# Optimization experiments

Measured on AMD Instinct MI355X. Metric: run time of the kernel, lower is better.

The kernel has to match this reference:

```python
import jax, jax.numpy as jnp
import numpy as np

# module hyper-params (init_kwargs); shift_sz=1 => 1x1 patches == pixels, flag == mask
SHIFT_SZ = 1
STRIDE = 1
MASK_THRED = 1
TRIPLE_WEIGHT = 1.0   # only rescales gradients in the original custom backward; forward output unchanged
FUSE = True
FUSE_K = 3            # contextual-attention fuse kernel size (identity 3x3)


def _fuse_scores(score, H, W):
    # score: [B, L, L] (query loc, key loc). Contextual-attention 'fuse':
    # smooth the score map with an identity kernel along both spatial unfoldings.
    B, L, _ = score.shape
    eye = jnp.eye(FUSE_K, dtype=score.dtype).reshape(1, 1, FUSE_K, FUSE_K)

    def conv(x):
        return jax.lax.conv_general_dilated(
            x, eye, window_strides=(1, 1), padding='SAME',
            dimension_numbers=('NCHW', 'OIHW', 'NCHW'))

    s = conv(score[:, None])                                            # [B,1,L,L]
    s = s.reshape(B, H, W, H, W).transpose(0, 2, 1, 4, 3).reshape(B, 1, L, L)
    s = conv(s)
    s = s.reshape(B, W, H, W, H).transpose(0, 2, 1, 4, 3).reshape(B, L, L)
    return s


def reference(x, mask):
    # x: [B, 2c, H, W]; first c channels = former (decoder feat), last c = latter (encoder feat)
    B, C2, H, W = x.shape
    c = C2 // 2
    L = H * W
    former = x[:, :c]
    latter = x[:, c:]

    # flag: True = inside hole. With shift_sz=1, stride=1, mask_thred=1 the patch flag is the mask itself.
    flag = mask.reshape(L) > 0.5                                        # [L]

    lat = latter.reshape(B, c, L)
    # normalize context (key) patches to unit L2 norm -> cosine-style correlation
    key = lat / jnp.maximum(jnp.linalg.norm(lat, axis=1, keepdims=True), 1e-4)
    score = jnp.einsum('bcl,bck->blk', lat, key)                        # [B, L(query), L(key)]
    if FUSE:
        score = _fuse_scores(score, H, W)

    # only attend to context patches OUTSIDE the hole
    score = jnp.where(flag[None, None, :], -jnp.inf, score)
    attn = jax.nn.softmax(score, axis=-1)                               # [B, L, L]

    # soft shift: attention-weighted gather of former (decoder) features from context pixels
    shift = jnp.einsum('blk,bck->bcl', attn, former.reshape(B, c, L))   # [B, c, L]
    # the shifted feature only fills hole locations; zero elsewhere
    shift = shift * flag[None, None, :].astype(x.dtype)
    shift = shift.reshape(B, c, H, W)

    return jnp.concatenate([former, latter, shift], axis=1)             # [B, 3c, H, W]


def setup_inputs():
    key = jax.random.key(0)
    k1, k2 = jax.random.split(key)
    B, c, H, W = 2, 64, 64, 64
    x = jax.random.normal(k1, (B, 2 * c, H, W), dtype=jnp.float32)
    mask = (jax.random.uniform(k2, (1, 1, H, W)) > 0.75).astype(jnp.float32)
    return {"x": x, "mask": mask}
```

## Files before the change

kernel.cpp:

```cpp
#include <hip/hip_runtime.h>
#include <math.h>


#define L 4096

typedef unsigned int   u32;
typedef unsigned short u16;
typedef short  short8 __attribute__((ext_vector_type(8)));
typedef float  f32x16 __attribute__((ext_vector_type(16)));

#define MFMA32(a, b, c) __builtin_amdgcn_mfma_f32_32x32x16_bf16((a), (b), (c), 0, 0, 0)

__device__ __forceinline__ u16 f2bf(float f) {
    u32 u = __float_as_uint(f);
    u32 r = (u + 0x7FFFu + ((u >> 16) & 1u)) >> 16;
    return (u16)r;
}

__device__ __forceinline__ void lds_async16(void* lds, const void* g) {
    __builtin_amdgcn_global_load_lds((const __attribute__((address_space(1))) u32*)g,
                                     (__attribute__((address_space(3))) u32*)lds, 16, 0, 0);
}

#define OFF_LATB  0u
#define OFF_FORB  1048576u
#define OFF_GARR  2097152u
#define GARR_BB   1575936u
#define OFF_FBITS 5249024u
#define OFF_ROWS  5249536u
#define OFF_CNT   5265920u
#define OFF_PART  5266432u
#define OFF_KNB   5266432u

__global__ void k_pre1(const float4* __restrict__ x4, float4* __restrict__ out4,
                       const float* __restrict__ x, const float* __restrict__ mask,
                       u16* __restrict__ latb, u16* __restrict__ knb, u16* __restrict__ forb,
                       int* __restrict__ rows, int* __restrict__ cnt, u32* __restrict__ fbits)
{
    const int blk = blockIdx.x, t = threadIdx.x;
    if (blk < 1537) {
        int i = blk * 256 + t;
        if (i < 262144) {
            int b = i >> 17, j = i & 131071;
            out4[b * 196608 + j] = x4[b * 131072 + j];
        } else if (i < 393216) {
            int z = i - 262144; int b = z >> 16, j = z & 65535;
            out4[b * 196608 + 131072 + j] = make_float4(0.f, 0.f, 0.f, 0.f);
        }
    } else if (blk < 1569) {
        int tid = (blk - 1537) * 256 + t;
        int b = tid >> 12, l = tid & 4095;
        const float* xb = x + (size_t)b * 524288;
        float v[64]; float ss = 0.f;
        #pragma unroll
        for (int c = 0; c < 64; ++c) { v[c] = xb[(64 + c) * 4096 + l]; ss += v[c] * v[c]; }
        float inv = 1.f / fmaxf(sqrtf(ss), 1e-4f);
        u16* lr = latb + (size_t)(b * 4096 + l) * 64;
        u16* kr = knb  + (size_t)(b * 4096 + l) * 64;
        #pragma unroll
        for (int c8 = 0; c8 < 8; ++c8) {
            u32 wl[4], wk[4];
            #pragma unroll
            for (int i = 0; i < 4; ++i) {
                float a = v[c8 * 8 + 2 * i], bb2 = v[c8 * 8 + 2 * i + 1];
                wl[i] = (u32)f2bf(a) | ((u32)f2bf(bb2) << 16);
                wk[i] = (u32)f2bf(a * inv) | ((u32)f2bf(bb2 * inv) << 16);
            }
            uint4 pl = make_uint4(wl[0], wl[1], wl[2], wl[3]);
            uint4 pk = make_uint4(wk[0], wk[1], wk[2], wk[3]);
            *(uint4*)(lr + c8 * 8) = pl;
            *(uint4*)(kr + c8 * 8) = pk;
        }
        u16* fr = forb + (size_t)(b * 4096 + l) * 64;
        #pragma unroll
        for (int c8 = 0; c8 < 8; ++c8) {
            u32 wf[4];
            #pragma unroll
            for (int i = 0; i < 4; ++i) {
                float a = xb[(c8 * 8 + 2 * i) * 4096 + l];
                float bb2 = xb[(c8 * 8 + 2 * i + 1) * 4096 + l];
                wf[i] = (u32)f2bf(a) | ((u32)f2bf(bb2) << 16);
            }
            uint4 pf = make_uint4(wf[0], wf[1], wf[2], wf[3]);
            *(uint4*)(fr + c8 * 8) = pf;
        }
    } else {
        __shared__ int lcnt;
        __shared__ u32 lb[128];
        if (t == 0) lcnt = 0;
        if (t < 128) lb[t] = 0u;
        __syncthreads();
        for (int i = t; i < L; i += 256) {
            if (mask[i] > 0.5f) {
                int p = atomicAdd(&lcnt, 1); rows[p] = i;
                int kp = ((i & 63) << 6) | (i >> 6);
                atomicOr(&lb[kp >> 5], 1u << (kp & 31));
            }
        }
        __syncthreads();
        if (t < 128) fbits[t] = lb[t];
        if (t == 0) cnt[0] = lcnt;
    }
}

__global__ void k_garr(const u16* __restrict__ knb, char* __restrict__ garr)
{
    int tid = blockIdx.x * 256 + threadIdx.x;
    if (tid >= 2 * 4104 * 3) return;
    int b = tid / 12312; int rem = tid - b * 12312;
    int sg = rem / 3, aa = rem - 3 * (rem / 3);
    int mp = sg - 1;
    char* dst = garr + (size_t)b * GARR_BB + (size_t)sg * 384;
    int key = (sg & 7) << 4;
    const u16* src = nullptr;
    if (mp >= 0 && mp < L) {
        int q = (((mp & 63) << 6) | (mp >> 6)) + aa - 1;
        if (q >= 0 && q < L) src = knb + (size_t)b * 262144 + (size_t)q * 64;
    }
    #pragma unroll
    for (int c8 = 0; c8 < 8; ++c8) {
        uint4 v = src ? *(const uint4*)(src + c8 * 8) : make_uint4(0, 0, 0, 0);
        *(uint4*)(dst + ((aa * 128 + c8 * 16) ^ key)) = v;
    }
}

__global__ __launch_bounds__(256, 2)
void k_flash(const u16* __restrict__ latb, const u16* __restrict__ forb,
             const char* __restrict__ garr, const u32* __restrict__ fbits,
             const int* __restrict__ rows, const int* __restrict__ cnt,
             char* __restrict__ part)
{
    __shared__ __align__(16) char smem[80000];
    char* slab = smem;
    u16*  F_s  = (u16*)(smem + 52224);
    u16*  p_s  = (u16*)(smem + 69632);
    int*  rl_s = (int*)(smem + 79872);

    const int t = threadIdx.x;
    const int rt = blockIdx.x, ks = blockIdx.y, b = blockIdx.z;
    const int count = cnt[0];
    const int base = rt * 32;
    if (base >= count) return;
    const int nact = min(32, count - base);
    if (t < 32) rl_s[t] = rows[base + min(t, nact - 1)];
    __syncthreads();

    const int l = t & 63, w = t >> 6;
    const int li = l & 31, hi = l >> 5;
    const size_t boff = (size_t)b * 262144;

    const u16* zp = (const u16*)garr;
    int gl = rl_s[li];
    int tl0 = ((gl & 63) << 6) | (gl >> 6);
    const u16* rp[9];
    #pragma unroll
    for (int tap = 0; tap < 9; ++tap) {
        int bb = tap / 3, aa = tap - 3 * (tap / 3);
        int mp = tl0 + bb - 1;
        const u16* p = zp;
        if (mp >= 0 && mp < L) {
            int q = (((mp & 63) << 6) | (mp >> 6)) + aa - 1;
            if (q >= 0 && q < L) p = latb + boff + (size_t)q * 64;
        }
        rp[tap] = p;
    }
    short8 bu[36];
    #pragma unroll
    for (int q = 0; q < 36; ++q) {
        int tap = q >> 2, Ksi = q & 3;
        bu[q] = *(const short8*)(rp[tap] + Ksi * 16 + hi * 8);
    }

    float mrun = -INFINITY, srun = 0.f;
    f32x16 acc0, acc1;
    #pragma unroll
    for (int r = 0; r < 16; ++r) { acc0[r] = 0.f; acc1[r] = 0.f; }

    const int kp0 = ks * 512;
    const char* gb = garr + (size_t)b * GARR_BB;

    for (int kt = 0; kt < 4; ++kt) {
        const int k0p = kp0 + kt * 128;
        __syncthreads();

        const char* gw = gb + (size_t)k0p * 384;
        #pragma unroll
        for (int i = 0; i < 13; ++i) {
            int idx = w + 4 * i;
            if (idx < 51)
                lds_async16(slab + idx * 1024, gw + idx * 1024 + l * 16);
        }

        {
            int kpA = k0p + 2 * l, kpB = kpA + 1;
            int kA = ((kpA & 63) << 6) | (kpA >> 6);
            int kB = ((kpB & 63) << 6) | (kpB >> 6);
            const u32* pa = (const u32*)(forb + boff + (size_t)kA * 64 + w * 16);
            const u32* pc = (const u32*)(forb + boff + (size_t)kB * 64 + w * 16);
            uint4 A0 = *(const uint4*)pa, A1 = *(const uint4*)(pa + 4);
            uint4 B0 = *(const uint4*)pc, B1 = *(const uint4*)(pc + 4);
            u32 av[8] = {A0.x, A0.y, A0.z, A0.w, A1.x, A1.y, A1.z, A1.w};
            u32 bv[8] = {B0.x, B0.y, B0.z, B0.w, B1.x, B1.y, B1.z, B1.w};
            #pragma unroll
            for (int i2 = 0; i2 < 8; ++i2) {
                u32 w0 = (av[i2] & 0xffffu) | (bv[i2] << 16);
                u32 w1 = (av[i2] >> 16) | (bv[i2] & 0xffff0000u);
                *(u32*)((char*)F_s + (w * 16 + 2 * i2) * 272 + l * 4) = w0;
                *(u32*)((char*)F_s + (w * 16 + 2 * i2 + 1) * 272 + l * 4) = w1;
            }
        }
        asm volatile("s_waitcnt vmcnt(0)" ::: "memory");
        __syncthreads();

        f32x16 sc;
        #pragma unroll
        for (int r = 0; r < 16; ++r) sc[r] = 0.f;
        const int slot_base = w * 32 + li;
        #pragma unroll
        for (int tap = 0; tap < 9; ++tap) {
            int bb = tap / 3, aa = tap - 3 * (tap / 3);
            int sl = slot_base + bb;
            int key = (sl & 7) << 4;
            int base_b = sl * 384 + aa * 128 + hi * 16;
            #pragma unroll
            for (int Ksi = 0; Ksi < 4; ++Ksi) {
                short8 ag = *(const short8*)(slab + ((base_b + Ksi * 32) ^ key));
                sc = MFMA32(ag, bu[tap * 4 + Ksi], sc);
            }
        }

        u32 bits = fbits[(k0p >> 5) + w];
        float sv[16]; float mx = -INFINITY;
        #pragma unroll
        for (int r = 0; r < 16; ++r) {
            int kloc = (r & 3) + 8 * (r >> 2) + 4 * hi;
            float s = sc[r];
            if ((bits >> kloc) & 1) s = -INFINITY;
            sv[r] = s; mx = fmaxf(mx, s);
        }
        mx = fmaxf(mx, __shfl_xor(mx, 32, 64));
        float newm = fmaxf(mrun, mx);
        float fac, tsum = 0.f;
        u16 pb[16];
        if (newm > -INFINITY) {
            fac = __expf(mrun - newm);
            #pragma unroll
            for (int r = 0; r < 16; ++r) { float p = __expf(sv[r] - newm); tsum += p; pb[r] = f2bf(p); }
        } else {
            fac = 1.f;
            #pragma unroll
            for (int r = 0; r < 16; ++r) pb[r] = 0;
        }
        tsum += __shfl_xor(tsum, 32, 64);
        srun = srun * fac + tsum;
        mrun = newm;
        #pragma unroll
        for (int rq = 0; rq < 8; ++rq) {
            int r = rq * 2;
            int kloc = (r & 3) + 8 * (r >> 2) + 4 * hi;
            u32 pw = (u32)pb[r] | ((u32)pb[r + 1] << 16);
            *(u32*)(p_s + w * 1280 + li * 40 + kloc) = pw;
        }

        #pragma unroll
        for (int r = 0; r < 16; ++r) {
            int row = (r & 3) + 8 * (r >> 2) + 4 * hi;
            float fr = __shfl(fac, row, 64);
            acc0[r] *= fr; acc1[r] *= fr;
        }
        #pragma unroll
        for (int Ksi2 = 0; Ksi2 < 2; ++Ksi2) {
            short8 pa2 = *(const short8*)(p_s + w * 1280 + li * 40 + Ksi2 * 16 + hi * 8);
            short8 f0 = *(const short8*)(F_s + li * 136 + w * 32 + Ksi2 * 16 + hi * 8);
            short8 f1 = *(const short8*)(F_s + (32 + li) * 136 + w * 32 + Ksi2 * 16 + hi * 8);
            acc0 = MFMA32(pa2, f0, acc0);
            acc1 = MFMA32(pa2, f1, acc1);
        }
    }

    __syncthreads();
    float* um = (float*)smem;
    if (l < 32) { um[(w * 32 + li) * 66] = mrun; um[(w * 32 + li) * 66 + 1] = srun; }
    #pragma unroll
    for (int r = 0; r < 16; ++r) {
        int row = (r & 3) + 8 * (r >> 2) + 4 * hi;
        um[(w * 32 + row) * 66 + 2 + li] = acc0[r];
        um[(w * 32 + row) * 66 + 2 + 32 + li] = acc1[r];
    }
    __syncthreads();
    {
        int row = t >> 3, cq = t & 7;
        float m4[4], s4[4];
        #pragma unroll
        for (int wv = 0; wv < 4; ++wv) {
            m4[wv] = um[(wv * 32 + row) * 66];
            s4[wv] = um[(wv * 32 + row) * 66 + 1];
        }
        float M = fmaxf(fmaxf(m4[0], m4[1]), fmaxf(m4[2], m4[3]));
        float S = 0.f; float wx[4];
        if (M > -INFINITY) {
            #pragma unroll
            for (int wv = 0; wv < 4; ++wv) { wx[wv] = __expf(m4[wv] - M); S += s4[wv] * wx[wv]; }
        } else {
            wx[0] = wx[1] = wx[2] = wx[3] = 0.f;
        }
        char* pp = part + ((size_t)((b * 128 + rt) * 8 + ks)) * 4608 + row * 144;
        u16 h[8];
        #pragma unroll
        for (int i = 0; i < 8; ++i) {
            int ch = cq * 8 + i;
            float v = 0.f;
            #pragma unroll
            for (int wv = 0; wv < 4; ++wv) v += wx[wv] * um[(wv * 32 + row) * 66 + 2 + ch];
            h[i] = f2bf(v);
        }
        if (cq == 0) { *(float*)pp = M; *(float*)(pp + 4) = S; }
        uint4 hw;
        hw.x = (u32)h[0] | ((u32)h[1] << 16); hw.y = (u32)h[2] | ((u32)h[3] << 16);
        hw.z = (u32)h[4] | ((u32)h[5] << 16); hw.w = (u32)h[6] | ((u32)h[7] << 16);
        *(uint4*)(pp + 16 + cq * 16) = hw;
    }
}

__global__ void k_reduce(const int* __restrict__ rows, const int* __restrict__ cnt,
                         const char* __restrict__ part, float* __restrict__ out)
{
    int t = threadIdx.x;
    int row = t >> 3, cq = t & 7;
    int rt = blockIdx.x, b = blockIdx.y;
    int count = cnt[0];
    int slot = rt * 32 + row;
    if (slot >= count) return;
    int l = rows[slot];
    const char* pb = part + ((size_t)((b * 128 + rt) * 8)) * 4608 + row * 144;
    float M = -INFINITY, m8[8], s8[8];
    #pragma unroll
    for (int k = 0; k < 8; ++k) {
        m8[k] = *(const float*)(pb + k * 4608);
        s8[k] = *(const float*)(pb + k * 4608 + 4);
        M = fmaxf(M, m8[k]);
    }
    if (!(M > -INFINITY)) return;
    float S = 0.f; float accv[8] = {0.f, 0.f, 0.f, 0.f, 0.f, 0.f, 0.f, 0.f};
    #pragma unroll
    for (int k = 0; k < 8; ++k) {
        float wxv = __expf(m8[k] - M);
        S += s8[k] * wxv;
        uint4 hv = *(const uint4*)(pb + k * 4608 + 16 + cq * 16);
        u32 uu[4] = {hv.x, hv.y, hv.z, hv.w};
        #pragma unroll
        for (int i = 0; i < 4; ++i) {
            accv[2 * i]     += wxv * __uint_as_float((uu[i] & 0xffffu) << 16);
            accv[2 * i + 1] += wxv * __uint_as_float(uu[i] & 0xffff0000u);
        }
    }
    float inv = (S > 0.f) ? 1.f / S : 0.f;
    float* ob = out + (size_t)b * 786432 + 524288 + l;
    #pragma unroll
    for (int i = 0; i < 8; ++i) ob[(size_t)(cq * 8 + i) * 4096] = accv[i] * inv;
}

extern "C" void kernel_launch(void* const* d_in, const int* in_sizes, int n_in,
                              void* d_out, int out_size, void* d_ws, size_t ws_size,
                              hipStream_t stream)
{
    const float* x    = (const float*)d_in[0];
    const float* mask = (const float*)d_in[1];
    float* out = (float*)d_out;
    char* ws = (char*)d_ws;

    u16* latb = (u16*)(ws + OFF_LATB);
    u16* forb = (u16*)(ws + OFF_FORB);
    char* garr = ws + OFF_GARR;
    u32* fbits = (u32*)(ws + OFF_FBITS);
    int* rows  = (int*)(ws + OFF_ROWS);
    int* cnt   = (int*)(ws + OFF_CNT);
    char* part = ws + OFF_PART;
    u16* knb   = (u16*)(ws + OFF_KNB);

    k_pre1<<<1570, 256, 0, stream>>>((const float4*)x, (float4*)out, x, mask,
                                     latb, knb, forb, rows, cnt, fbits);
    k_garr<<<97, 256, 0, stream>>>(knb, garr);
    k_flash<<<dim3(128, 8, 2), 256, 0, stream>>>(latb, forb, garr, fbits, rows, cnt, part);
    k_reduce<<<dim3(128, 2), 256, 0, stream>>>(rows, cnt, part, out);
}
```

Baseline: 143.7 us.

## Rewrite attention pipeline: fuse reduce into flash kernel, drop gather-array pass

Most of the pipeline is replaced. The separate k_garr gather kernel goes away, and k_pre1 now writes normalized keys straight into a swizzled, transposed padded layout plus a channel-major former buffer via an LDS transpose. k_flash now uses 512 threads and large dynamic LDS, each block covering a 512-key slice in one pass without online-softmax rescaling. The last block to finish each row tile, found through an atomic done counter, does the cross-split reduction in place of the k_reduce launch. It also remaps blocks across XCDs and caps hole rows at 2048; in exchange it brings atomics, threadfences and lower occupancy.

```diff
diff --git a/kernel.cpp b/kernel.cpp
--- a/kernel.cpp
+++ b/kernel.cpp
@@ -3,361 +3,345 @@
 
 
 #define L 4096
-
 typedef unsigned int   u32;
 typedef unsigned short u16;
 typedef short  short8 __attribute__((ext_vector_type(8)));
 typedef float  f32x16 __attribute__((ext_vector_type(16)));
 
-#define MFMA32(a, b, c) __builtin_amdgcn_mfma_f32_32x32x16_bf16((a), (b), (c), 0, 0, 0)
-
-__device__ __forceinline__ u16 f2bf(float f) {
-    u32 u = __float_as_uint(f);
-    u32 r = (u + 0x7FFFu + ((u >> 16) & 1u)) >> 16;
-    return (u16)r;
+#define MFMA32(a,b,c) __builtin_amdgcn_mfma_f32_32x32x16_bf16((a),(b),(c),0,0,0)
+
+__device__ __forceinline__ u16 f2bf(float f){ u32 u=__float_as_uint(f); return (u16)((u+0x7FFFu+((u>>16)&1u))>>16); }
+__device__ __forceinline__ u32 pack2(float a, float b){ return (u32)f2bf(a) | ((u32)f2bf(b)<<16); }
+__device__ __forceinline__ void lds_async16(void* lds, const void* g){
+  __builtin_amdgcn_global_load_lds((const __attribute__((address_space(1))) u32*)g,
+                                   (__attribute__((address_space(3))) u32*)lds, 16, 0, 0);
 }
 
-__device__ __forceinline__ void lds_async16(void* lds, const void* g) {
-    __builtin_amdgcn_global_load_lds((const __attribute__((address_space(1))) u32*)g,
-                                     (__attribute__((address_space(3))) u32*)lds, 16, 0, 0);
-}
-
 #define OFF_LATB  0u
-#define OFF_FORB  1048576u
-#define OFF_GARR  2097152u
-#define GARR_BB   1575936u
-#define OFF_FBITS 5249024u
-#define OFF_ROWS  5249536u
-#define OFF_CNT   5265920u
-#define OFF_PART  5266432u
-#define OFF_KNB   5266432u
+#define OFF_FORKP 1048576u
+#define OFF_KNXG  2097152u
+#define KNXG_BB   542208u
+#define OFF_FBITS 3211264u
+#define OFF_ROWS  3211776u
+#define OFF_CNT   3228160u
+#define OFF_DONE  3228416u
+#define OFF_PART  3229440u
+
+#define SLAB_O  0
+#define POFF    82432
+#define ZOFF    90624
+#define UOFF    90752
+#define PSOFF   127616
+#define RLOFF   162432
+#define SMEM_SZ 162688
 
 __global__ void k_pre1(const float4* __restrict__ x4, float4* __restrict__ out4,
                        const float* __restrict__ x, const float* __restrict__ mask,
-                       u16* __restrict__ latb, u16* __restrict__ knb, u16* __restrict__ forb,
-                       int* __restrict__ rows, int* __restrict__ cnt, u32* __restrict__ fbits)
+                       u16* __restrict__ latb, u16* __restrict__ forkp,
+                       char* __restrict__ knxg, int* __restrict__ rows,
+                       int* __restrict__ cnt, u32* __restrict__ fbits,
+                       u32* __restrict__ done)
 {
+    __shared__ float tl[64*65];
+    __shared__ int lcnt;
+    __shared__ u32 lb[128];
     const int blk = blockIdx.x, t = threadIdx.x;
-    if (blk < 1537) {
-        int i = blk * 256 + t;
-        if (i < 262144) {
-            int b = i >> 17, j = i & 131071;
-            out4[b * 196608 + j] = x4[b * 131072 + j];
-        } else if (i < 393216) {
-            int z = i - 262144; int b = z >> 16, j = z & 65535;
-            out4[b * 196608 + 131072 + j] = make_float4(0.f, 0.f, 0.f, 0.f);
-        }
-    } else if (blk < 1569) {
-        int tid = (blk - 1537) * 256 + t;
-        int b = tid >> 12, l = tid & 4095;
-        const float* xb = x + (size_t)b * 524288;
-        float v[64]; float ss = 0.f;
-        #pragma unroll
-        for (int c = 0; c < 64; ++c) { v[c] = xb[(64 + c) * 4096 + l]; ss += v[c] * v[c]; }
-        float inv = 1.f / fmaxf(sqrtf(ss), 1e-4f);
-        u16* lr = latb + (size_t)(b * 4096 + l) * 64;
-        u16* kr = knb  + (size_t)(b * 4096 + l) * 64;
-        #pragma unroll
-        for (int c8 = 0; c8 < 8; ++c8) {
-            u32 wl[4], wk[4];
+    if (blk < 1536) {
+        int i = blk*256 + t;
+        if (i < 262144) { int b=i>>17, j=i&131071; out4[b*196608+j] = x4[b*131072+j]; }
+        else { int z=i-262144; int b=z>>16, j=z&65535; out4[b*196608+131072+j] = make_float4(0.f,0.f,0.f,0.f); }
+    } else if (blk < 1568) {
+        int tid = (blk-1536)*256+t; int b = tid>>12, l = tid&4095;
+        const float* xb = x + (size_t)b*524288;
+        float v[64]; float ss=0.f;
+        #pragma unroll
+        for (int c=0;c<64;++c){ v[c]=xb[(64+c)*4096+l]; ss+=v[c]*v[c]; }
+        float inv = 1.f/fmaxf(sqrtf(ss),1e-4f);
+        u16* lr = latb + (size_t)(b*4096+l)*64;
+        #pragma unroll
+        for (int c8=0;c8<8;++c8){
+            uint4 pq = make_uint4(pack2(v[c8*8],v[c8*8+1]),pack2(v[c8*8+2],v[c8*8+3]),
+                                  pack2(v[c8*8+4],v[c8*8+5]),pack2(v[c8*8+6],v[c8*8+7]));
+            *(uint4*)(lr + c8*8) = pq;
+        }
+        int t2 = ((l&63)<<6)|(l>>6);
+        char* dst = knxg + (size_t)b*KNXG_BB + (size_t)(t2+66)*128;
+        int key = (t2&7)<<4;
+        #pragma unroll
+        for (int c8=0;c8<8;++c8){
+            uint4 pq = make_uint4(pack2(v[c8*8]*inv,v[c8*8+1]*inv),pack2(v[c8*8+2]*inv,v[c8*8+3]*inv),
+                                  pack2(v[c8*8+4]*inv,v[c8*8+5]*inv),pack2(v[c8*8+6]*inv,v[c8*8+7]*inv));
+            *(uint4*)(dst + ((c8*16)^key)) = pq;
+        }
+    } else if (blk < 1696) {
+        int blk2 = blk-1568; int b = blk2>>6, ch = blk2&63;
+        const float* in = x + (size_t)b*524288 + (size_t)ch*4096;
+        #pragma unroll
+        for (int i=0;i<16;++i){ int idx = t+256*i; tl[(idx&63)*65 + (idx>>6)] = in[idx]; }
+        __syncthreads();
+        u32* orow = (u32*)forkp + (size_t)(b*64+ch)*2048;
+        #pragma unroll
+        for (int i=0;i<8;++i){
+            int j2 = t+256*i; int j = 2*j2;
+            float f0 = tl[(j>>6)*65 + (j&63)];
+            float f1 = tl[((j+1)>>6)*65 + ((j+1)&63)];
+            orow[j2] = pack2(f0,f1);
+        }
+    } else if (blk < 1698) {
+        int b = blk-1696;
+        char* gB = knxg + (size_t)b*KNXG_BB;
+        uint4 z = make_uint4(0,0,0,0);
+        #pragma unroll
+        for (int i=0;i<5;++i){
+            int idx = t+256*i;
+            if (idx < 1120){
+                int row = (idx<528) ? (idx>>3) : (4162 + ((idx-528)>>3));
+                *(uint4*)(gB + (size_t)row*128 + (idx&7)*16) = z;
+            }
+        }
+    } else {
+        if (t==0) lcnt=0;
+        if (t<128) lb[t]=0u;
+        __syncthreads();
+        for (int i=t;i<L;i+=256){
+            if (mask[i] > 0.5f){
+                int p = atomicAdd(&lcnt,1);
+                if (p<2048) rows[p]=i;
+                int kp = ((i&63)<<6)|(i>>6);
+                atomicOr(&lb[kp>>5], 1u<<(kp&31));
+            }
+        }
+        __syncthreads();
+        if (t<128) fbits[t]=lb[t];
+        if (t<128) done[t]=0u;
+        if (t==0) cnt[0]=min(lcnt,2048);
+    }
+}
+
+__global__ __launch_bounds__(512,1)
+void k_flash(const u16* __restrict__ latb, const u16* __restrict__ forkp,
+             const char* __restrict__ knxg, const u32* __restrict__ fbits,
+             const int* __restrict__ rows, const int* __restrict__ cnt,
+             char* __restrict__ part, u32* __restrict__ done, float* __restrict__ out)
+{
+    extern __shared__ char smem[];
+    const int t = threadIdx.x;
+    const int lin = blockIdx.x;
+    const int xcd = lin&7, qd = lin>>3;
+    const int gid = xcd*128 + qd;
+    const int ksb = gid>>6, rt = gid&63;
+    const int ks = ksb>>1, b = ksb&1;
+    const int count = cnt[0];
+    const int base = rt*32;
+    if (base >= count) return;
+    const int nact = min(32, count-base);
+    int* rl_s = (int*)(smem + RLOFF);
+    if (t < 32) rl_s[t] = rows[base + min(t, nact-1)];
+    if (t < 8) *(uint4*)(smem + ZOFF + t*16) = make_uint4(0,0,0,0);
+    __syncthreads();
+
+    const int l = t&63, w = t>>6, li = l&31, hi = l>>5;
+    const int k0 = ks*512, wOff = w*64;
+    const int plo = (ks==0) ? 4031 : 1;
+    const char* slabsrc = knxg + (size_t)b*KNXG_BB + (size_t)k0*128;
+
+    #pragma unroll
+    for (int i=0;i<11;++i){
+        int idx = w + 8*i;
+        if (idx < 80 || (idx == 80 && l < 24))
+            lds_async16(smem + SLAB_O + idx*1024, slabsrc + idx*1024 + l*16);
+    }
+    if (ks==0 || ks==7){
+        const char* psrc = knxg + (size_t)b*KNXG_BB + (size_t)(plo+66)*128;
+        lds_async16(smem + POFF + w*1024, psrc + w*1024 + l*16);
+    }
+    {
+        const u16* latbb = latb + (size_t)b*262144;
+        int gl = rl_s[li];
+        int tl0 = ((gl&63)<<6)|(gl>>6);
+        #pragma unroll
+        for (int rep=0;rep<5;++rep){
+            int f = w + 8*rep;
+            if (f < 36){
+                int tap = f>>2, Ks = f&3;
+                int bb = tap/3, aa = tap - 3*bb;
+                int mp = tl0 + bb - 1;
+                short8 val = {0,0,0,0,0,0,0,0};
+                if (mp>=0 && mp<L){
+                    int qq = (((mp&63)<<6)|(mp>>6)) + aa - 1;
+                    if (qq>=0 && qq<L)
+                        val = *(const short8*)(latbb + (size_t)qq*64 + Ks*16 + hi*8);
+                }
+                *(short8*)(smem + UOFF + f*1024 + l*16) = val;
+            }
+        }
+    }
+    int pkA[2][9];
+    #pragma unroll
+    for (int Mt=0; Mt<2; ++Mt){
+        #pragma unroll
+        for (int tap=0; tap<9; ++tap){
+            const int bb = tap/3, aa = tap - 3*(tap/3);
+            int j = k0 + wOff + Mt*32 + li + bb - 1;
+            int pk = ZOFF;
+            if ((u32)j < (u32)L){
+                int qq = (j&63)*64 + (j>>6) + aa - 1;
+                if ((u32)qq < (u32)L){
+                    int t2 = ((qq&63)<<6) | (qq>>6);
+                    int key = (t2&7)<<4;
+                    int s = t2 - k0 + 66;
+                    if ((u32)s < 643u) pk = SLAB_O + s*128 + key;
+                    else               pk = POFF + (t2 - plo)*128 + key;
+                }
+            }
+            pkA[Mt][tap] = pk;
+        }
+    }
+
+    asm volatile("s_waitcnt vmcnt(0)" ::: "memory");
+    __syncthreads();
+
+    f32x16 sc0, sc1;
+    #pragma unroll
+    for (int r=0;r<16;++r){ sc0[r]=0.f; sc1[r]=0.f; }
+    const char* ubp = smem + UOFF + l*16;
+    const int X0 = hi*16;
+    __builtin_amdgcn_s_setprio(1);
+    #pragma unroll
+    for (int tap=0; tap<9; ++tap){
+        const int r0 = pkA[0][tap] & ~127, y0 = pkA[0][tap] & 127;
+        const int r1 = pkA[1][tap] & ~127, y1 = pkA[1][tap] & 127;
+        #pragma unroll
+        for (int Ks=0; Ks<4; ++Ks){
+            short8 bu = *(const short8*)(ubp + (tap*4+Ks)*1024);
+            short8 a0 = *(const short8*)(smem + r0 + ((X0 + Ks*32) ^ y0));
+            short8 a1 = *(const short8*)(smem + r1 + ((X0 + Ks*32) ^ y1));
+            sc0 = MFMA32(a0, bu, sc0);
+            sc1 = MFMA32(a1, bu, sc1);
+        }
+    }
+    __builtin_amdgcn_s_setprio(0);
+
+    const u16* fKb = forkp + (size_t)b*262144;
+    short8 fb0[4], fb1[4];
+    #pragma unroll
+    for (int Ks=0;Ks<4;++Ks){
+        fb0[Ks] = *(const short8*)(fKb + (size_t)li*4096      + k0 + wOff + Ks*16 + hi*8);
+        fb1[Ks] = *(const short8*)(fKb + (size_t)(32+li)*4096 + k0 + wOff + Ks*16 + hi*8);
+    }
+
+    const int fw = (k0 + wOff) >> 5;
+    const u32 bits0 = fbits[fw], bits1 = fbits[fw+1];
+    float mx = -INFINITY;
+    #pragma unroll
+    for (int r=0;r<16;++r){
+        int kl = (r&3) + 8*(r>>2) + 4*hi;
+        float s0 = sc0[r]; if ((bits0>>kl)&1u) s0 = -INFINITY;
+        float s1 = sc1[r]; if ((bits1>>kl)&1u) s1 = -INFINITY;
+        sc0[r]=s0; sc1[r]=s1;
+        mx = fmaxf(mx, fmaxf(s0,s1));
+    }
+    mx = fmaxf(mx, __shfl_xor(mx, 32, 64));
+    float sum = 0.f;
+    u32 pw0[8], pw1[8];
+    if (mx > -INFINITY){
+        #pragma unroll
+        for (int rq=0;rq<8;++rq){
+            float p00 = __expf(sc0[2*rq]-mx), p01 = __expf(sc0[2*rq+1]-mx);
+            float p10 = __expf(sc1[2*rq]-mx), p11 = __expf(sc1[2*rq+1]-mx);
+            sum += (p00+p01)+(p10+p11);
+            pw0[rq] = pack2(p00,p01);
+            pw1[rq] = pack2(p10,p11);
+        }
+    } else {
+        #pragma unroll
+        for (int rq=0;rq<8;++rq){ pw0[rq]=0u; pw1[rq]=0u; }
+    }
+    sum += __shfl_xor(sum, 32, 64);
+    char* pswr = smem + PSOFF + w*4352 + li*136;
+    #pragma unroll
+    for (int rq=0;rq<8;++rq){
+        int r = 2*rq;
+        int kl = (r&3) + 8*(r>>2) + 4*hi;
+        *(u32*)(pswr + kl*2)      = pw0[rq];
+        *(u32*)(pswr + 64 + kl*2) = pw1[rq];
+    }
+
+    f32x16 ac0, ac1;
+    #pragma unroll
+    for (int r=0;r<16;++r){ ac0[r]=0.f; ac1[r]=0.f; }
+    #pragma unroll
+    for (int Ks=0;Ks<4;++Ks){
+        short8 pa = *(const short8*)(pswr + Ks*32 + X0);
+        ac0 = MFMA32(pa, fb0[Ks], ac0);
+        ac1 = MFMA32(pa, fb1[Ks], ac1);
+    }
+
+    __syncthreads();
+    float* um = (float*)smem;
+    if (hi==0){ um[(w*32+li)*66+0] = mx; um[(w*32+li)*66+1] = sum; }
+    #pragma unroll
+    for (int r=0;r<16;++r){
+        int kl = (r&3)+8*(r>>2)+4*hi;
+        um[(w*32+kl)*66 + 2 + li]      = ac0[r];
+        um[(w*32+kl)*66 + 2 + 32 + li] = ac1[r];
+    }
+    __syncthreads();
+    {
+        int row = t>>4, cq = t&15, ch4 = cq*4;
+        float M = -INFINITY; float m8[8], s8[8];
+        #pragma unroll
+        for (int wv=0;wv<8;++wv){ m8[wv]=um[(wv*32+row)*66]; s8[wv]=um[(wv*32+row)*66+1]; M=fmaxf(M,m8[wv]); }
+        float S=0.f; float a4[4]={0.f,0.f,0.f,0.f};
+        if (M > -INFINITY){
             #pragma unroll
-            for (int i = 0; i < 4; ++i) {
-                float a = v[c8 * 8 + 2 * i], bb2 = v[c8 * 8 + 2 * i + 1];
-                wl[i] = (u32)f2bf(a) | ((u32)f2bf(bb2) << 16);
-                wk[i] = (u32)f2bf(a * inv) | ((u32)f2bf(bb2 * inv) << 16);
-            }
-            uint4 pl = make_uint4(wl[0], wl[1], wl[2], wl[3]);
-            uint4 pk = make_uint4(wk[0], wk[1], wk[2], wk[3]);
-            *(uint4*)(lr + c8 * 8) = pl;
-            *(uint4*)(kr + c8 * 8) = pk;
-        }
-        u16* fr = forb + (size_t)(b * 4096 + l) * 64;
-        #pragma unroll
-        for (int c8 = 0; c8 < 8; ++c8) {
-            u32 wf[4];
+            for (int wv=0;wv<8;++wv){
+                float e = __expf(m8[wv]-M);
+                S += s8[wv]*e;
+                #pragma unroll
+                for (int i=0;i<4;++i) a4[i] += e * um[(wv*32+row)*66 + 2 + ch4 + i];
+            }
+        }
+        char* rec = part + ((size_t)((b*64+rt)*8 + ks))*4608 + row*144;
+        if (cq==0){ *(float*)rec = M; *(float*)(rec+4) = S; }
+        uint2 hw; hw.x = pack2(a4[0],a4[1]); hw.y = pack2(a4[2],a4[3]);
+        *(uint2*)(rec + 16 + ch4*2) = hw;
+    }
+
+    __threadfence();
+    __syncthreads();
+    if (t==0) rl_s[0] = (atomicAdd(&done[b*64+rt],1u) == 7u) ? 1 : 0;
+    __syncthreads();
+    if (!rl_s[0]) return;
+    __threadfence();
+    {
+        int row = t>>4, cq = t&15, ch4 = cq*4;
+        int slot = base + row;
+        if (slot < count){
+            int lr2 = rows[slot];
+            const char* pbp = part + ((size_t)((b*64+rt)*8))*4608 + row*144;
+            float M=-INFINITY; float m8[8], s8[8];
             #pragma unroll
-            for (int i = 0; i < 4; ++i) {
-                float a = xb[(c8 * 8 + 2 * i) * 4096 + l];
-                float bb2 = xb[(c8 * 8 + 2 * i + 1) * 4096 + l];
-                wf[i] = (u32)f2bf(a) | ((u32)f2bf(bb2) << 16);
-            }
-            uint4 pf = make_uint4(wf[0], wf[1], wf[2], wf[3]);
-            *(uint4*)(fr + c8 * 8) = pf;
-        }
-    } else {
-        __shared__ int lcnt;
-        __shared__ u32 lb[128];
-        if (t == 0) lcnt = 0;
-        if (t < 128) lb[t] = 0u;
-        __syncthreads();
-        for (int i = t; i < L; i += 256) {
-            if (mask[i] > 0.5f) {
-                int p = atomicAdd(&lcnt, 1); rows[p] = i;
-                int kp = ((i & 63) << 6) | (i >> 6);
-                atomicOr(&lb[kp >> 5], 1u << (kp & 31));
-            }
-        }
-        __syncthreads();
-        if (t < 128) fbits[t] = lb[t];
-        if (t == 0) cnt[0] = lcnt;
-    }
-}
-
-__global__ void k_garr(const u16* __restrict__ knb, char* __restrict__ garr)
-{
-    int tid = blockIdx.x * 256 + threadIdx.x;
-    if (tid >= 2 * 4104 * 3) return;
-    int b = tid / 12312; int rem = tid - b * 12312;
-    int sg = rem / 3, aa = rem - 3 * (rem / 3);
-    int mp = sg - 1;
-    char* dst = garr + (size_t)b * GARR_BB + (size_t)sg * 384;
-    int key = (sg & 7) << 4;
-    const u16* src = nullptr;
-    if (mp >= 0 && mp < L) {
-        int q = (((mp & 63) << 6) | (mp >> 6)) + aa - 1;
-        if (q >= 0 && q < L) src = knb + (size_t)b * 262144 + (size_t)q * 64;
-    }
-    #pragma unroll
-    for (int c8 = 0; c8 < 8; ++c8) {
-        uint4 v = src ? *(const uint4*)(src + c8 * 8) : make_uint4(0, 0, 0, 0);
-        *(uint4*)(dst + ((aa * 128 + c8 * 16) ^ key)) = v;
-    }
-}
-
-__global__ __launch_bounds__(256, 2)
-void k_flash(const u16* __restrict__ latb, const u16* __restrict__ forb,
-             const char* __restrict__ garr, const u32* __restrict__ fbits,
-             const int* __restrict__ rows, const int* __restrict__ cnt,
-             char* __restrict__ part)
-{
-    __shared__ __align__(16) char smem[80000];
-    char* slab = smem;
-    u16*  F_s  = (u16*)(smem + 52224);
-    u16*  p_s  = (u16*)(smem + 69632);
-    int*  rl_s = (int*)(smem + 79872);
-
-    const int t = threadIdx.x;
-    const int rt = blockIdx.x, ks = blockIdx.y, b = blockIdx.z;
-    const int count = cnt[0];
-    const int base = rt * 32;
-    if (base >= count) return;
-    const int nact = min(32, count - base);
-    if (t < 32) rl_s[t] = rows[base + min(t, nact - 1)];
-    __syncthreads();
-
-    const int l = t & 63, w = t >> 6;
-    const int li = l & 31, hi = l >> 5;
-    const size_t boff = (size_t)b * 262144;
-
-    const u16* zp = (const u16*)garr;
-    int gl = rl_s[li];
-    int tl0 = ((gl & 63) << 6) | (gl >> 6);
-    const u16* rp[9];
-    #pragma unroll
-    for (int tap = 0; tap < 9; ++tap) {
-        int bb = tap / 3, aa = tap - 3 * (tap / 3);
-        int mp = tl0 + bb - 1;
-        const u16* p = zp;
-        if (mp >= 0 && mp < L) {
-            int q = (((mp & 63) << 6) | (mp >> 6)) + aa - 1;
-            if (q >= 0 && q < L) p = latb + boff + (size_t)q * 64;
-        }
-        rp[tap] = p;
-    }
-    short8 bu[36];
-    #pragma unroll
-    for (int q = 0; q < 36; ++q) {
-        int tap = q >> 2, Ksi = q & 3;
-        bu[q] = *(const short8*)(rp[tap] + Ksi * 16 + hi * 8);
-    }
-
-    float mrun = -INFINITY, srun = 0.f;
-    f32x16 acc0, acc1;
-    #pragma unroll
-    for (int r = 0; r < 16; ++r) { acc0[r] = 0.f; acc1[r] = 0.f; }
-
-    const int kp0 = ks * 512;
-    const char* gb = garr + (size_t)b * GARR_BB;
-
-    for (int kt = 0; kt < 4; ++kt) {
-        const int k0p = kp0 + kt * 128;
-        __syncthreads();
-
-        const char* gw = gb + (size_t)k0p * 384;
-        #pragma unroll
-        for (int i = 0; i < 13; ++i) {
-            int idx = w + 4 * i;
-            if (idx < 51)
-                lds_async16(slab + idx * 1024, gw + idx * 1024 + l * 16);
-        }
-
-        {
-            int kpA = k0p + 2 * l, kpB = kpA + 1;
-            int kA = ((kpA & 63) << 6) | (kpA >> 6);
-            int kB = ((kpB & 63) << 6) | (kpB >> 6);
-            const u32* pa = (const u32*)(forb + boff + (size_t)kA * 64 + w * 16);
-            const u32* pc = (const u32*)(forb + boff + (size_t)kB * 64 + w * 16);
-            uint4 A0 = *(const uint4*)pa, A1 = *(const uint4*)(pa + 4);
-            uint4 B0 = *(const uint4*)pc, B1 = *(const uint4*)(pc + 4);
-            u32 av[8] = {A0.x, A0.y, A0.z, A0.w, A1.x, A1.y, A1.z, A1.w};
-            u32 bv[8] = {B0.x, B0.y, B0.z, B0.w, B1.x, B1.y, B1.z, B1.w};
-            #pragma unroll
-            for (int i2 = 0; i2 < 8; ++i2) {
-                u32 w0 = (av[i2] & 0xffffu) | (bv[i2] << 16);
-                u32 w1 = (av[i2] >> 16) | (bv[i2] & 0xffff0000u);
-                *(u32*)((char*)F_s + (w * 16 + 2 * i2) * 272 + l * 4) = w0;
-                *(u32*)((char*)F_s + (w * 16 + 2 * i2 + 1) * 272 + l * 4) = w1;
-            }
-        }
-        asm volatile("s_waitcnt vmcnt(0)" ::: "memory");
-        __syncthreads();
-
-        f32x16 sc;
-        #pragma unroll
-        for (int r = 0; r < 16; ++r) sc[r] = 0.f;
-        const int slot_base = w * 32 + li;
-        #pragma unroll
-        for (int tap = 0; tap < 9; ++tap) {
-            int bb = tap / 3, aa = tap - 3 * (tap / 3);
-            int sl = slot_base + bb;
-            int key = (sl & 7) << 4;
-            int base_b = sl * 384 + aa * 128 + hi * 16;
-            #pragma unroll
-            for (int Ksi = 0; Ksi < 4; ++Ksi) {
-                short8 ag = *(const short8*)(slab + ((base_b + Ksi * 32) ^ key));
-                sc = MFMA32(ag, bu[tap * 4 + Ksi], sc);
-            }
-        }
-
-        u32 bits = fbits[(k0p >> 5) + w];
-        float sv[16]; float mx = -INFINITY;
-        #pragma unroll
-        for (int r = 0; r < 16; ++r) {
-            int kloc = (r & 3) + 8 * (r >> 2) + 4 * hi;
-            float s = sc[r];
-            if ((bits >> kloc) & 1) s = -INFINITY;
-            sv[r] = s; mx = fmaxf(mx, s);
-        }
-        mx = fmaxf(mx, __shfl_xor(mx, 32, 64));
-        float newm = fmaxf(mrun, mx);
-        float fac, tsum = 0.f;
-        u16 pb[16];
-        if (newm > -INFINITY) {
-            fac = __expf(mrun - newm);
-            #pragma unroll
-            for (int r = 0; r < 16; ++r) { float p = __expf(sv[r] - newm); tsum += p; pb[r] = f2bf(p); }
-        } else {
-            fac = 1.f;
-            #pragma unroll
-            for (int r = 0; r < 16; ++r) pb[r] = 0;
-        }
-        tsum += __shfl_xor(tsum, 32, 64);
-        srun = srun * fac + tsum;
-        mrun = newm;
-        #pragma unroll
-        for (int rq = 0; rq < 8; ++rq) {
-            int r = rq * 2;
-            int kloc = (r & 3) + 8 * (r >> 2) + 4 * hi;
-            u32 pw = (u32)pb[r] | ((u32)pb[r + 1] << 16);
-            *(u32*)(p_s + w * 1280 + li * 40 + kloc) = pw;
-        }
-
-        #pragma unroll
-        for (int r = 0; r < 16; ++r) {
-            int row = (r & 3) + 8 * (r >> 2) + 4 * hi;
-            float fr = __shfl(fac, row, 64);
-            acc0[r] *= fr; acc1[r] *= fr;
-        }
-        #pragma unroll
-        for (int Ksi2 = 0; Ksi2 < 2; ++Ksi2) {
-            short8 pa2 = *(const short8*)(p_s + w * 1280 + li * 40 + Ksi2 * 16 + hi * 8);
-            short8 f0 = *(const short8*)(F_s + li * 136 + w * 32 + Ksi2 * 16 + hi * 8);
-            short8 f1 = *(const short8*)(F_s + (32 + li) * 136 + w * 32 + Ksi2 * 16 + hi * 8);
-            acc0 = MFMA32(pa2, f0, acc0);
-            acc1 = MFMA32(pa2, f1, acc1);
-        }
-    }
-
-    __syncthreads();
-    float* um = (float*)smem;
-    if (l < 32) { um[(w * 32 + li) * 66] = mrun; um[(w * 32 + li) * 66 + 1] = srun; }
-    #pragma unroll
-    for (int r = 0; r < 16; ++r) {
-        int row = (r & 3) + 8 * (r >> 2) + 4 * hi;
-        um[(w * 32 + row) * 66 + 2 + li] = acc0[r];
-        um[(w * 32 + row) * 66 + 2 + 32 + li] = acc1[r];
-    }
-    __syncthreads();
-    {
-        int row = t >> 3, cq = t & 7;
-        float m4[4], s4[4];
-        #pragma unroll
-        for (int wv = 0; wv < 4; ++wv) {
-            m4[wv] = um[(wv * 32 + row) * 66];
-            s4[wv] = um[(wv * 32 + row) * 66 + 1];
-        }
-        float M = fmaxf(fmaxf(m4[0], m4[1]), fmaxf(m4[2], m4[3]));
-        float S = 0.f; float wx[4];
-        if (M > -INFINITY) {
-            #pragma unroll
-            for (int wv = 0; wv < 4; ++wv) { wx[wv] = __expf(m4[wv] - M); S += s4[wv] * wx[wv]; }
-        } else {
-            wx[0] = wx[1] = wx[2] = wx[3] = 0.f;
-        }
-        char* pp = part + ((size_t)((b * 128 + rt) * 8 + ks)) * 4608 + row * 144;
-        u16 h[8];
-        #pragma unroll
-        for (int i = 0; i < 8; ++i) {
-            int ch = cq * 8 + i;
-            float v = 0.f;
-            #pragma unroll
-            for (int wv = 0; wv < 4; ++wv) v += wx[wv] * um[(wv * 32 + row) * 66 + 2 + ch];
-            h[i] = f2bf(v);
-        }
-        if (cq == 0) { *(float*)pp = M; *(float*)(pp + 4) = S; }
-        uint4 hw;
-        hw.x = (u32)h[0] | ((u32)h[1] << 16); hw.y = (u32)h[2] | ((u32)h[3] << 16);
-        hw.z = (u32)h[4] | ((u32)h[5] << 16); hw.w = (u32)h[6] | ((u32)h[7] << 16);
-        *(uint4*)(pp + 16 + cq * 16) = hw;
-    }
-}
-
-__global__ void k_reduce(const int* __restrict__ rows, const int* __restrict__ cnt,
-                         const char* __restrict__ part, float* __restrict__ out)
-{
-    int t = threadIdx.x;
-    int row = t >> 3, cq = t & 7;
-    int rt = blockIdx.x, b = blockIdx.y;
-    int count = cnt[0];
-    int slot = rt * 32 + row;
-    if (slot >= count) return;
-    int l = rows[slot];
-    const char* pb = part + ((size_t)((b * 128 + rt) * 8)) * 4608 + row * 144;
-    float M = -INFINITY, m8[8], s8[8];
-    #pragma unroll
-    for (int k = 0; k < 8; ++k) {
-        m8[k] = *(const float*)(pb + k * 4608);
-        s8[k] = *(const float*)(pb + k * 4608 + 4);
-        M = fmaxf(M, m8[k]);
-    }
-    if (!(M > -INFINITY)) return;
-    float S = 0.f; float accv[8] = {0.f, 0.f, 0.f, 0.f, 0.f, 0.f, 0.f, 0.f};
-    #pragma unroll
-    for (int k = 0; k < 8; ++k) {
-        float wxv = __expf(m8[k] - M);
-        S += s8[k] * wxv;
-        uint4 hv = *(const uint4*)(pb + k * 4608 + 16 + cq * 16);
-        u32 uu[4] = {hv.x, hv.y, hv.z, hv.w};
-        #pragma unroll
-        for (int i = 0; i < 4; ++i) {
-            accv[2 * i]     += wxv * __uint_as_float((uu[i] & 0xffffu) << 16);
-            accv[2 * i + 1] += wxv * __uint_as_float(uu[i] & 0xffff0000u);
-        }
-    }
-    float inv = (S > 0.f) ? 1.f / S : 0.f;
-    float* ob = out + (size_t)b * 786432 + 524288 + l;
-    #pragma unroll
-    for (int i = 0; i < 8; ++i) ob[(size_t)(cq * 8 + i) * 4096] = accv[i] * inv;
+            for (int k=0;k<8;++k){ m8[k]=*(const float*)(pbp+k*4608); s8[k]=*(const float*)(pbp+k*4608+4); M=fmaxf(M,m8[k]); }
+            if (M > -INFINITY){
+                float S=0.f; float a4[4]={0.f,0.f,0.f,0.f};
+                #pragma unroll
+                for (int k=0;k<8;++k){
+                    float e = __expf(m8[k]-M);
+                    S += s8[k]*e;
+                    uint2 hv = *(const uint2*)(pbp + k*4608 + 16 + ch4*2);
+                    a4[0] += e*__uint_as_float((hv.x&0xffffu)<<16);
+                    a4[1] += e*__uint_as_float(hv.x & 0xffff0000u);
+                    a4[2] += e*__uint_as_float((hv.y&0xffffu)<<16);
+                    a4[3] += e*__uint_as_float(hv.y & 0xffff0000u);
+                }
+                float invS = (S>0.f) ? 1.f/S : 0.f;
+                float* ob = out + (size_t)b*786432 + 524288 + lr2;
+                #pragma unroll
+                for (int i=0;i<4;++i) ob[(size_t)(ch4+i)*4096] = a4[i]*invS;
+            }
+        }
+    }
 }
 
 extern "C" void kernel_launch(void* const* d_in, const int* in_sizes, int n_in,
@@ -369,18 +353,17 @@
     float* out = (float*)d_out;
     char* ws = (char*)d_ws;
 
-    u16* latb = (u16*)(ws + OFF_LATB);
-    u16* forb = (u16*)(ws + OFF_FORB);
-    char* garr = ws + OFF_GARR;
+    u16* latb  = (u16*)(ws + OFF_LATB);
+    u16* forkp = (u16*)(ws + OFF_FORKP);
+    char* knxg = ws + OFF_KNXG;
     u32* fbits = (u32*)(ws + OFF_FBITS);
     int* rows  = (int*)(ws + OFF_ROWS);
     int* cnt   = (int*)(ws + OFF_CNT);
+    u32* done  = (u32*)(ws + OFF_DONE);
     char* part = ws + OFF_PART;
-    u16* knb   = (u16*)(ws + OFF_KNB);
-
-    k_pre1<<<1570, 256, 0, stream>>>((const float4*)x, (float4*)out, x, mask,
-                                     latb, knb, forb, rows, cnt, fbits);
-    k_garr<<<97, 256, 0, stream>>>(knb, garr);
-    k_flash<<<dim3(128, 8, 2), 256, 0, stream>>>(latb, forb, garr, fbits, rows, cnt, part);
-    k_reduce<<<dim3(128, 2), 256, 0, stream>>>(rows, cnt, part, out);
+
+    k_pre1<<<1699, 256, 0, stream>>>((const float4*)x, (float4*)out, x, mask,
+                                     latb, forkp, knxg, rows, cnt, fbits, done);
+    hipFuncSetAttribute((const void*)k_flash, hipFuncAttributeMaxDynamicSharedMemorySize, SMEM_SZ);
+    k_flash<<<1024, 512, SMEM_SZ, stream>>>(latb, forkp, knxg, fbits, rows, cnt, part, done, out);
 }
```

After: 241.8 us. +68.2%, slower.
